# Optimization experiments

Measured on AMD Instinct MI355X. Metric: run time of the kernel, lower is better.

The kernel has to match this reference:

```python
import jax, jax.numpy as jnp
import numpy as np

N_NODES = 50000
N_EDGES = 800000
D = 128
L = 3


def setup_inputs() -> dict:
    key = jax.random.key(0)
    ks = jax.random.split(key, 16)
    x = jax.random.normal(ks[0], (N_NODES, D), dtype=jnp.float32)
    edge_index = jax.random.randint(ks[1], (2, N_EDGES), 0, N_NODES, dtype=jnp.int32)
    # ensure every node has at least one incoming edge (degree > 0)
    edge_index = edge_index.at[1, :N_NODES].set(jnp.arange(N_NODES, dtype=jnp.int32))
    edge_attr = jax.random.normal(ks[2], (N_EDGES, 1), dtype=jnp.float32)
    s = 1.0 / np.sqrt(D)
    lin_w = jax.random.normal(ks[3], (L, 1, D), dtype=jnp.float32)          # edge_dim=1 -> D
    lin_b = jax.random.normal(ks[4], (L, D), dtype=jnp.float32) * s
    eps = jnp.zeros((L,), dtype=jnp.float32)                                 # initial_eps = 0, trainable
    w1 = jax.random.normal(ks[5], (L, D, D), dtype=jnp.float32) * s
    b1 = jax.random.normal(ks[6], (L, D), dtype=jnp.float32) * s
    w2 = jax.random.normal(ks[7], (L, D, D), dtype=jnp.float32) * s
    b2 = jax.random.normal(ks[8], (L, D), dtype=jnp.float32) * s
    d_cat = D + L * D
    final_w = jax.random.normal(ks[9], (d_cat, D), dtype=jnp.float32) / np.sqrt(d_cat)
    final_b = jax.random.normal(ks[10], (D,), dtype=jnp.float32) * s
    return {"x": x, "edge_index": edge_index, "edge_attr": edge_attr,
            "lin_w": lin_w, "lin_b": lin_b, "eps": eps,
            "w1": w1, "b1": b1, "w2": w2, "b2": b2,
            "final_w": final_w, "final_b": final_b}


def reference(x, edge_index, edge_attr, lin_w, lin_b, eps, w1, b1, w2, b2, final_w, final_b):
    src, tgt = edge_index[0], edge_index[1]
    n = x.shape[0]
    # degree of target nodes (float), shape [N, 1]
    deg = jax.ops.segment_sum(jnp.ones(src.shape[0], x.dtype), tgt, num_segments=n)[:, None]
    xs = [x]
    h = x
    for l in range(L):
        e = edge_attr @ lin_w[l] + lin_b[l]                  # [E, D] edge-feature projection
        msg = jax.nn.relu(h[src] + e)                        # gather + fuse + relu
        agg = jax.ops.segment_sum(msg, tgt, num_segments=n)  # scatter-add
        out = agg / deg + (1.0 + eps[l]) * h                 # degree-normalize + eps-residual
        h = jax.nn.relu(out @ w1[l] + b1[l]) @ w2[l] + b2[l] # 2-layer MLP (no BN, no dropout)
        xs.append(h)
    cat = jnp.concatenate(xs, axis=-1)                       # [N, D + L*D]
    return cat @ final_w + final_b
```

## Files before the change

kernel.cpp:

```cpp
#include <hip/hip_runtime.h>

#define NN 50000
#define NE 800000
#define DIM 128
#define NLAYERS 3

typedef __attribute__((ext_vector_type(8))) short bf16x8;
typedef __attribute__((ext_vector_type(4))) float f32x4;

__device__ __forceinline__ unsigned short f2bf_hi(float f) {
    unsigned int u = __float_as_uint(f);
    u += 0x7FFF + ((u >> 16) & 1);
    return (unsigned short)(u >> 16);
}
__device__ __forceinline__ float bf2f(unsigned short u) {
    return __uint_as_float(((unsigned int)u) << 16);
}

__global__ __launch_bounds__(256) void rank_kernel(const int* __restrict__ tgt,
                                                   int* __restrict__ counts,
                                                   int* __restrict__ rank, int E) {
    int base = (blockIdx.x * 256 + threadIdx.x) * 4;
    if (base >= E) return;
    int4 t = *(const int4*)(tgt + base);
    int4 r;
    r.x = atomicAdd(&counts[t.x], 1);
    r.y = atomicAdd(&counts[t.y], 1);
    r.z = atomicAdd(&counts[t.z], 1);
    r.w = atomicAdd(&counts[t.w], 1);
    *(int4*)(rank + base) = r;
}

__global__ __launch_bounds__(256) void scan_partial_kernel(const int* __restrict__ counts,
                                                           int* __restrict__ psum, int n) {
    __shared__ int ws[4];
    int b = blockIdx.x, t = threadIdx.x;
    int idx = b * 1024 + t * 4;
    int v = 0;
    if (idx < n) {
        int4 c = *(const int4*)(counts + idx);
        v = c.x + c.y + c.z + c.w;
    }
#pragma unroll
    for (int o = 32; o > 0; o >>= 1) v += __shfl_xor(v, o);
    int lane = t & 63, wid = t >> 6;
    if (lane == 0) ws[wid] = v;
    __syncthreads();
    if (t == 0) psum[b] = ws[0] + ws[1] + ws[2] + ws[3];
}

__global__ __launch_bounds__(64) void scan_small_kernel(const int* __restrict__ psum,
                                                        int* __restrict__ pbase,
                                                        int* __restrict__ offsets,
                                                        int nb, int n) {
    int lane = threadIdx.x;
    int v = (lane < nb) ? psum[lane] : 0;
    int incl = v;
#pragma unroll
    for (int o = 1; o < 64; o <<= 1) {
        int t = __shfl_up(incl, o);
        if (lane >= o) incl += t;
    }
    if (lane < nb) pbase[lane] = incl - v;
    if (lane == 63) offsets[n] = incl;
}

__global__ __launch_bounds__(256) void scan_apply_kernel(const int* __restrict__ counts,
                                                         const int* __restrict__ pbase,
                                                         int* __restrict__ offsets, int n) {
    __shared__ int ws[4];
    int b = blockIdx.x, t = threadIdx.x;
    int lane = t & 63, wid = t >> 6;
    int idx = b * 1024 + t * 4;
    int4 c = make_int4(0, 0, 0, 0);
    if (idx < n) c = *(const int4*)(counts + idx);
    int tsum = c.x + c.y + c.z + c.w;
    int incl = tsum;
#pragma unroll
    for (int o = 1; o < 64; o <<= 1) {
        int tt = __shfl_up(incl, o);
        if (lane >= o) incl += tt;
    }
    if (lane == 63) ws[wid] = incl;
    __syncthreads();
    int wbase = pbase[b];
    for (int w = 0; w < wid; w++) wbase += ws[w];
    if (idx < n) {
        int e0 = wbase + incl - tsum;
        int4 o;
        o.x = e0;
        o.y = e0 + c.x;
        o.z = o.y + c.y;
        o.w = o.z + c.z;
        *(int4*)(offsets + idx) = o;
    }
}

__global__ __launch_bounds__(256) void scatter2_kernel(
    const int* __restrict__ src, const int* __restrict__ tgt,
    const float* __restrict__ ea, const int* __restrict__ rank,
    const int* __restrict__ offsets, int2* __restrict__ sedge, int E) {
    int base = (blockIdx.x * 256 + threadIdx.x) * 4;
    if (base >= E) return;
    int4 s = *(const int4*)(src + base);
    int4 t = *(const int4*)(tgt + base);
    int4 r = *(const int4*)(rank + base);
    float4 a = *(const float4*)(ea + base);
    sedge[offsets[t.x] + r.x] = make_int2(s.x << 8, __float_as_int(a.x));
    sedge[offsets[t.y] + r.y] = make_int2(s.y << 8, __float_as_int(a.y));
    sedge[offsets[t.z] + r.z] = make_int2(s.z << 8, __float_as_int(a.z));
    sedge[offsets[t.w] + r.w] = make_int2(s.w << 8, __float_as_int(a.w));
}

__global__ __launch_bounds__(256) void xcvt_kernel(const float* __restrict__ x,
                                                   unsigned short* __restrict__ xb, int n) {
    int i = (blockIdx.x * 256 + threadIdx.x) * 4;
    if (i >= n) return;
    float4 v = *(const float4*)(x + i);
    ushort4 o;
    o.x = f2bf_hi(v.x); o.y = f2bf_hi(v.y);
    o.z = f2bf_hi(v.z); o.w = f2bf_hi(v.w);
    *(ushort4*)(xb + i) = o;
}

__global__ __launch_bounds__(256) void agg_kernel(
    const unsigned short* __restrict__ hprev, const int* __restrict__ offs,
    const int2* __restrict__ sedge,
    const float* __restrict__ lw, const float* __restrict__ lb,
    const float* __restrict__ epsp, int layer,
    unsigned short* __restrict__ aggh, unsigned short* __restrict__ aggl, int N) {
    int wv = threadIdx.x >> 6;
    int node = blockIdx.x * 4 + wv;
    if (node >= N) return;
    int lane = threadIdx.x & 63;
    int q = lane >> 4, r = lane & 15;
    int d0 = r * 8;
    float lwv[8], lbv[8];
    *(float4*)&lwv[0] = *(const float4*)(lw + d0);
    *(float4*)&lwv[4] = *(const float4*)(lw + d0 + 4);
    *(float4*)&lbv[0] = *(const float4*)(lb + d0);
    *(float4*)&lbv[4] = *(const float4*)(lb + d0 + 4);
    int s0 = offs[node], s1 = offs[node + 1];
    int cnt = s1 - s0;
    float a[8];
#pragma unroll
    for (int c = 0; c < 8; c++) a[c] = 0.f;

    const char* hbase = (const char*)hprev + r * 16;

    int idx = s0 + q;
    int2 e0 = sedge[min(idx, s1 - 1)];
    int2 e1 = sedge[min(idx + 4, s1 - 1)];
    int2 e2 = sedge[min(idx + 8, s1 - 1)];
    uint4 h0 = *(const uint4*)(hbase + (unsigned)e0.x);
    uint4 h1 = *(const uint4*)(hbase + (unsigned)e1.x);

    for (int it = idx; it < s1; it += 4) {
        uint4 h2 = *(const uint4*)(hbase + (unsigned)e2.x);
        int2 e3 = sedge[min(it + 12, s1 - 1)];
        float wgt = __int_as_float(e0.y);
        unsigned uu[4] = {h0.x, h0.y, h0.z, h0.w};
#pragma unroll
        for (int c = 0; c < 4; c++) {
            float f0 = __uint_as_float(uu[c] << 16);
            float f1 = __uint_as_float(uu[c] & 0xffff0000u);
            a[2 * c]     += fmaxf(f0 + fmaf(wgt, lwv[2 * c], lbv[2 * c]), 0.f);
            a[2 * c + 1] += fmaxf(f1 + fmaf(wgt, lwv[2 * c + 1], lbv[2 * c + 1]), 0.f);
        }
        e0 = e1; e1 = e2; e2 = e3;
        h0 = h1; h1 = h2;
    }

#pragma unroll
    for (int c = 0; c < 8; c++) {
        a[c] += __shfl_xor(a[c], 16);
        a[c] += __shfl_xor(a[c], 32);
    }

    if (q == 0) {
        float inv = 1.f / (float)cnt;
        float ge = 1.f + epsp[layer];
        uint4 hs = *(const uint4*)(hbase + ((unsigned)node << 8));
        unsigned su[4] = {hs.x, hs.y, hs.z, hs.w};
        unsigned short hh[8], hl[8];
#pragma unroll
        for (int c = 0; c < 4; c++) {
            float f0 = __uint_as_float(su[c] << 16);
            float f1 = __uint_as_float(su[c] & 0xffff0000u);
            float v0 = a[2 * c] * inv + ge * f0;
            float v1 = a[2 * c + 1] * inv + ge * f1;
            unsigned short h0v = f2bf_hi(v0), h1v = f2bf_hi(v1);
            hh[2 * c] = h0v; hh[2 * c + 1] = h1v;
            hl[2 * c] = f2bf_hi(v0 - bf2f(h0v));
            hl[2 * c + 1] = f2bf_hi(v1 - bf2f(h1v));
        }
        unsigned short* ph = aggh + (size_t)node * DIM + d0;
        unsigned short* pl = aggl + (size_t)node * DIM + d0;
        *(ushort4*)ph       = *(const ushort4*)&hh[0];
        *(ushort4*)(ph + 4) = *(const ushort4*)&hh[4];
        *(ushort4*)pl       = *(const ushort4*)&hl[0];
        *(ushort4*)(pl + 4) = *(const ushort4*)&hl[4];
    }
}

__device__ __forceinline__ int packidx(int k, int c) {
    return (((k >> 5) << 3) + (c >> 4)) * 512 + (((k >> 3) & 3) << 7) + ((c & 15) << 3) + (k & 7);
}

__global__ __launch_bounds__(256) void wprep_kernel(
    const float* __restrict__ w1, const float* __restrict__ w2, const float* __restrict__ fw,
    unsigned short* __restrict__ w1t_h, unsigned short* __restrict__ w1t_l,
    unsigned short* __restrict__ w2t_h, unsigned short* __restrict__ w2t_l,
    unsigned short* __restrict__ fwt_h, unsigned short* __restrict__ fwt_l) {
    int gid = blockIdx.x * 256 + threadIdx.x;
    float v; int oidx;
    unsigned short *oh, *ol;
    if (gid < 49152) {
        int l = gid >> 14, rem = gid & 16383, k = rem >> 7, c = rem & 127;
        v = w1[gid]; oidx = l * 16384 + packidx(k, c); oh = w1t_h; ol = w1t_l;
    } else if (gid < 98304) {
        int g = gid - 49152;
        int l = g >> 14, rem = g & 16383, k = rem >> 7, c = rem & 127;
        v = w2[g]; oidx = l * 16384 + packidx(k, c); oh = w2t_h; ol = w2t_l;
    } else if (gid < 163840) {
        int g = gid - 98304;
        int k = g >> 7, c = g & 127;
        v = fw[g]; oidx = packidx(k, c); oh = fwt_h; ol = fwt_l;
    } else return;
    unsigned short h = f2bf_hi(v);
    float lo = v - bf2f(h);
    oh[oidx] = h;
    ol[oidx] = f2bf_hi(lo);
}

#define HSTR 136

__global__ __launch_bounds__(256, 4) void mlp_fused(
    const unsigned short* __restrict__ ah_g, const unsigned short* __restrict__ al_g,
    const unsigned short* __restrict__ w1h, const unsigned short* __restrict__ w1l,
    const float* __restrict__ b1,
    const unsigned short* __restrict__ w2h, const unsigned short* __restrict__ w2l,
    const float* __restrict__ b2,
    unsigned short* __restrict__ out, int N) {
    __shared__ unsigned short s_hh[64 * HSTR], s_hl[64 * HSTR];
    int tid = threadIdx.x;
    int lane = tid & 63, w = tid >> 6;
    int q = lane >> 4, lr = lane & 15;
    int wr = w >> 1, wc = w & 1;
    int n0 = blockIdx.x * 64;
    int nb0 = n0 + wc * 32 + lr;

    f32x4 acc[4][2];
#pragma unroll
    for (int i = 0; i < 4; i++)
#pragma unroll
        for (int j = 0; j < 2; j++) acc[i][j] = (f32x4)(0.f);

#pragma unroll
    for (int k0 = 0; k0 < 128; k0 += 32) {
        bf16x8 Bh[2], Bl[2];
#pragma unroll
        for (int j = 0; j < 2; j++) {
            size_t ro = (size_t)min(nb0 + j * 16, N - 1) * DIM + k0 + q * 8;
            Bh[j] = *(const bf16x8*)(ah_g + ro);
            Bl[j] = *(const bf16x8*)(al_g + ro);
        }
#pragma unroll
        for (int i = 0; i < 4; i++) {
            size_t co = ((size_t)((k0 >> 5) * 8 + wr * 4 + i) << 9) + lane * 8;
            bf16x8 Ah = *(const bf16x8*)(w1h + co);
            bf16x8 Al = *(const bf16x8*)(w1l + co);
#pragma unroll
            for (int j = 0; j < 2; j++) {
                acc[i][j] = __builtin_amdgcn_mfma_f32_16x16x32_bf16(Ah, Bh[j], acc[i][j], 0, 0, 0);
                acc[i][j] = __builtin_amdgcn_mfma_f32_16x16x32_bf16(Ah, Bl[j], acc[i][j], 0, 0, 0);
                acc[i][j] = __builtin_amdgcn_mfma_f32_16x16x32_bf16(Al, Bh[j], acc[i][j], 0, 0, 0);
            }
        }
    }

#pragma unroll
    for (int i = 0; i < 4; i++) {
        int hc0 = wr * 64 + i * 16 + q * 4;
        float4 bv = *(const float4*)(b1 + hc0);
        float bvr[4] = {bv.x, bv.y, bv.z, bv.w};
#pragma unroll
        for (int j = 0; j < 2; j++) {
            int nl = wc * 32 + j * 16 + lr;
            unsigned short hh[4], hl[4];
#pragma unroll
            for (int r = 0; r < 4; r++) {
                float v = fmaxf(acc[i][j][r] + bvr[r], 0.f);
                unsigned short h = f2bf_hi(v);
                hh[r] = h;
                hl[r] = f2bf_hi(v - bf2f(h));
            }
            *(ushort4*)&s_hh[nl * HSTR + hc0] = *(const ushort4*)&hh[0];
            *(ushort4*)&s_hl[nl * HSTR + hc0] = *(const ushort4*)&hl[0];
        }
    }
    __syncthreads();

#pragma unroll
    for (int i = 0; i < 4; i++)
#pragma unroll
        for (int j = 0; j < 2; j++) acc[i][j] = (f32x4)(0.f);

#pragma unroll
    for (int k0 = 0; k0 < 128; k0 += 32) {
        bf16x8 Bh[2], Bl[2];
#pragma unroll
        for (int j = 0; j < 2; j++) {
            int so = (wc * 32 + j * 16 + lr) * HSTR + k0 + q * 8;
            Bh[j] = *(const bf16x8*)&s_hh[so];
            Bl[j] = *(const bf16x8*)&s_hl[so];
        }
#pragma unroll
        for (int i = 0; i < 4; i++) {
            size_t co = ((size_t)((k0 >> 5) * 8 + wr * 4 + i) << 9) + lane * 8;
            bf16x8 Ah = *(const bf16x8*)(w2h + co);
            bf16x8 Al = *(const bf16x8*)(w2l + co);
#pragma unroll
            for (int j = 0; j < 2; j++) {
                acc[i][j] = __builtin_amdgcn_mfma_f32_16x16x32_bf16(Ah, Bh[j], acc[i][j], 0, 0, 0);
                acc[i][j] = __builtin_amdgcn_mfma_f32_16x16x32_bf16(Ah, Bl[j], acc[i][j], 0, 0, 0);
                acc[i][j] = __builtin_amdgcn_mfma_f32_16x16x32_bf16(Al, Bh[j], acc[i][j], 0, 0, 0);
            }
        }
    }

#pragma unroll
    for (int i = 0; i < 4; i++) {
        int hc0 = wr * 64 + i * 16 + q * 4;
        float4 bv = *(const float4*)(b2 + hc0);
        float bvr[4] = {bv.x, bv.y, bv.z, bv.w};
#pragma unroll
        for (int j = 0; j < 2; j++) {
            int node = nb0 + j * 16;
            if (node < N) {
                unsigned short o[4];
#pragma unroll
                for (int r = 0; r < 4; r++) o[r] = f2bf_hi(acc[i][j][r] + bvr[r]);
                *(ushort4*)&out[(size_t)node * DIM + hc0] = *(const ushort4*)&o[0];
            }
        }
    }
}

__global__ __launch_bounds__(256, 4) void final_mfma(
    const unsigned short* __restrict__ a0, const unsigned short* __restrict__ a1,
    const unsigned short* __restrict__ a2, const unsigned short* __restrict__ a3,
    const unsigned short* __restrict__ wh, const unsigned short* __restrict__ wl,
    const float* __restrict__ bias, float* __restrict__ out, int N) {
    int tid = threadIdx.x;
    int lane = tid & 63, w = tid >> 6;
    int q = lane >> 4, lr = lane & 15;
    int wr = w >> 1, wc = w & 1;
    int n0 = blockIdx.x * 64;
    int nb0 = n0 + wc * 32 + lr;

    f32x4 acc[4][2];
#pragma unroll
    for (int i = 0; i < 4; i++)
#pragma unroll
        for (int j = 0; j < 2; j++) acc[i][j] = (f32x4)(0.f);

#pragma unroll
    for (int s = 0; s < 4; s++) {
        const unsigned short* asrc = (s == 0) ? a0 : (s == 1) ? a1 : (s == 2) ? a2 : a3;
#pragma unroll
        for (int kk = 0; kk < 128; kk += 32) {
            int k0 = s * 128 + kk;
            bf16x8 B[2];
#pragma unroll
            for (int j = 0; j < 2; j++) {
                size_t ro = (size_t)min(nb0 + j * 16, N - 1) * DIM + kk + q * 8;
                B[j] = *(const bf16x8*)(asrc + ro);
            }
#pragma unroll
            for (int i = 0; i < 4; i++) {
                size_t co = ((size_t)((k0 >> 5) * 8 + wr * 4 + i) << 9) + lane * 8;
                bf16x8 Ah = *(const bf16x8*)(wh + co);
                bf16x8 Al = *(const bf16x8*)(wl + co);
#pragma unroll
                for (int j = 0; j < 2; j++) {
                    acc[i][j] = __builtin_amdgcn_mfma_f32_16x16x32_bf16(Ah, B[j], acc[i][j], 0, 0, 0);
                    acc[i][j] = __builtin_amdgcn_mfma_f32_16x16x32_bf16(Al, B[j], acc[i][j], 0, 0, 0);
                }
            }
        }
    }

#pragma unroll
    for (int i = 0; i < 4; i++) {
        int hc0 = wr * 64 + i * 16 + q * 4;
        float4 bv = *(const float4*)(bias + hc0);
        float bvr[4] = {bv.x, bv.y, bv.z, bv.w};
#pragma unroll
        for (int j = 0; j < 2; j++) {
            int node = nb0 + j * 16;
            if (node < N) {
                float4 o;
                o.x = acc[i][j][0] + bvr[0];
                o.y = acc[i][j][1] + bvr[1];
                o.z = acc[i][j][2] + bvr[2];
                o.w = acc[i][j][3] + bvr[3];
                *(float4*)&out[(size_t)node * DIM + hc0] = o;
            }
        }
    }
}

extern "C" void kernel_launch(void* const* d_in, const int* in_sizes, int n_in,
                              void* d_out, int out_size, void* d_ws, size_t ws_size,
                              hipStream_t stream) {
    const float* x   = (const float*)d_in[0];
    const int* edge_index = (const int*)d_in[1];
    const float* ea  = (const float*)d_in[2];
    const float* lw  = (const float*)d_in[3];
    const float* lb  = (const float*)d_in[4];
    const float* eps = (const float*)d_in[5];
    const float* w1  = (const float*)d_in[6];
    const float* b1  = (const float*)d_in[7];
    const float* w2  = (const float*)d_in[8];
    const float* b2  = (const float*)d_in[9];
    const float* fw  = (const float*)d_in[10];
    const float* fb  = (const float*)d_in[11];
    float* out = (float*)d_out;

    const int N = NN, E = NE;
    const int* src = edge_index;
    const int* tgt = edge_index + E;
    const int NB = (N + 1023) / 1024;

    char* ws = (char*)d_ws;
    size_t off = 0;
    auto alloc = [&](size_t bytes) {
        void* p = ws + off;
        off += (bytes + 255) & ~(size_t)255;
        return p;
    };
    int*   counts  = (int*)alloc((size_t)N * 4);
    int*   offsets = (int*)alloc((size_t)(N + 1) * 4);
    int*   rank    = (int*)alloc((size_t)E * 4);
    int*   psum    = (int*)alloc((size_t)NB * 4);
    int*   pbase   = (int*)alloc((size_t)NB * 4);
    int2*  sedge   = (int2*)alloc((size_t)E * 8);
    unsigned short* w1t_h = (unsigned short*)alloc(49152 * 2);
    unsigned short* w1t_l = (unsigned short*)alloc(49152 * 2);
    unsigned short* w2t_h = (unsigned short*)alloc(49152 * 2);
    unsigned short* w2t_l = (unsigned short*)alloc(49152 * 2);
    unsigned short* fwt_h = (unsigned short*)alloc(65536 * 2);
    unsigned short* fwt_l = (unsigned short*)alloc(65536 * 2);
    unsigned short* xb    = (unsigned short*)alloc((size_t)N * DIM * 2);
    unsigned short* hbuf[3];
    for (int i = 0; i < 3; i++) hbuf[i] = (unsigned short*)alloc((size_t)N * DIM * 2);
    unsigned short* aggh = (unsigned short*)alloc((size_t)N * DIM * 2);
    unsigned short* aggl = (unsigned short*)alloc((size_t)N * DIM * 2);
    (void)ws_size; (void)in_sizes; (void)n_in; (void)out_size;

    hipMemsetAsync(counts, 0, (size_t)N * 4, stream);
    rank_kernel<<<(E / 4 + 255) / 256, 256, 0, stream>>>(tgt, counts, rank, E);
    wprep_kernel<<<640, 256, 0, stream>>>(w1, w2, fw, w1t_h, w1t_l, w2t_h, w2t_l, fwt_h, fwt_l);
    xcvt_kernel<<<(N * DIM / 4 + 255) / 256, 256, 0, stream>>>(x, xb, N * DIM);
    scan_partial_kernel<<<NB, 256, 0, stream>>>(counts, psum, N);
    scan_small_kernel<<<1, 64, 0, stream>>>(psum, pbase, offsets, NB, N);
    scan_apply_kernel<<<NB, 256, 0, stream>>>(counts, pbase, offsets, N);
    scatter2_kernel<<<(E / 4 + 255) / 256, 256, 0, stream>>>(src, tgt, ea, rank, offsets, sedge, E);

    const int GB = (N + 63) / 64;
    for (int l = 0; l < NLAYERS; l++) {
        const unsigned short* hin = (l == 0) ? xb : hbuf[l - 1];
        agg_kernel<<<(N + 3) / 4, 256, 0, stream>>>(hin, offsets, sedge,
            lw + l * DIM, lb + l * DIM, eps, l, aggh, aggl, N);
        mlp_fused<<<GB, 256, 0, stream>>>(
            aggh, aggl,
            w1t_h + l * 16384, w1t_l + l * 16384, b1 + l * DIM,
            w2t_h + l * 16384, w2t_l + l * 16384, b2 + l * DIM,
            hbuf[l], N);
    }
    final_mfma<<<GB, 256, 0, stream>>>(
        xb, hbuf[0], hbuf[1], hbuf[2], fwt_h, fwt_l, fb, out, N);
}
```

Measured before the change: 371.4 us.

## Fuse edge aggregation into MLP kernel via swizzled shared-memory tile

The separate aggregation kernel is merged into the per-layer MLP kernel. Each block now aggregates its 64 nodes straight into shared memory, using 16 threads per node and a 4-deep software pipeline over edges. This removes the global round trip of the hi/lo aggregated buffers and one launch per layer. The padded shared-memory stride is replaced with an XOR swizzle. The cost is that each node's edges are walked serially by one 16-lane group instead of four, so latency hiding and load balance across high-degree nodes may suffer, and occupancy is tied to the MLP's launch bounds.

```diff
diff --git a/kernel.cpp b/kernel.cpp
--- a/kernel.cpp
+++ b/kernel.cpp
@@ -121,86 +121,6 @@
     o.x = f2bf_hi(v.x); o.y = f2bf_hi(v.y);
     o.z = f2bf_hi(v.z); o.w = f2bf_hi(v.w);
     *(ushort4*)(xb + i) = o;
-}
-
-__global__ __launch_bounds__(256) void agg_kernel(
-    const unsigned short* __restrict__ hprev, const int* __restrict__ offs,
-    const int2* __restrict__ sedge,
-    const float* __restrict__ lw, const float* __restrict__ lb,
-    const float* __restrict__ epsp, int layer,
-    unsigned short* __restrict__ aggh, unsigned short* __restrict__ aggl, int N) {
-    int wv = threadIdx.x >> 6;
-    int node = blockIdx.x * 4 + wv;
-    if (node >= N) return;
-    int lane = threadIdx.x & 63;
-    int q = lane >> 4, r = lane & 15;
-    int d0 = r * 8;
-    float lwv[8], lbv[8];
-    *(float4*)&lwv[0] = *(const float4*)(lw + d0);
-    *(float4*)&lwv[4] = *(const float4*)(lw + d0 + 4);
-    *(float4*)&lbv[0] = *(const float4*)(lb + d0);
-    *(float4*)&lbv[4] = *(const float4*)(lb + d0 + 4);
-    int s0 = offs[node], s1 = offs[node + 1];
-    int cnt = s1 - s0;
-    float a[8];
-#pragma unroll
-    for (int c = 0; c < 8; c++) a[c] = 0.f;
-
-    const char* hbase = (const char*)hprev + r * 16;
-
-    int idx = s0 + q;
-    int2 e0 = sedge[min(idx, s1 - 1)];
-    int2 e1 = sedge[min(idx + 4, s1 - 1)];
-    int2 e2 = sedge[min(idx + 8, s1 - 1)];
-    uint4 h0 = *(const uint4*)(hbase + (unsigned)e0.x);
-    uint4 h1 = *(const uint4*)(hbase + (unsigned)e1.x);
-
-    for (int it = idx; it < s1; it += 4) {
-        uint4 h2 = *(const uint4*)(hbase + (unsigned)e2.x);
-        int2 e3 = sedge[min(it + 12, s1 - 1)];
-        float wgt = __int_as_float(e0.y);
-        unsigned uu[4] = {h0.x, h0.y, h0.z, h0.w};
-#pragma unroll
-        for (int c = 0; c < 4; c++) {
-            float f0 = __uint_as_float(uu[c] << 16);
-            float f1 = __uint_as_float(uu[c] & 0xffff0000u);
-            a[2 * c]     += fmaxf(f0 + fmaf(wgt, lwv[2 * c], lbv[2 * c]), 0.f);
-            a[2 * c + 1] += fmaxf(f1 + fmaf(wgt, lwv[2 * c + 1], lbv[2 * c + 1]), 0.f);
-        }
-        e0 = e1; e1 = e2; e2 = e3;
-        h0 = h1; h1 = h2;
-    }
-
-#pragma unroll
-    for (int c = 0; c < 8; c++) {
-        a[c] += __shfl_xor(a[c], 16);
-        a[c] += __shfl_xor(a[c], 32);
-    }
-
-    if (q == 0) {
-        float inv = 1.f / (float)cnt;
-        float ge = 1.f + epsp[layer];
-        uint4 hs = *(const uint4*)(hbase + ((unsigned)node << 8));
-        unsigned su[4] = {hs.x, hs.y, hs.z, hs.w};
-        unsigned short hh[8], hl[8];
-#pragma unroll
-        for (int c = 0; c < 4; c++) {
-            float f0 = __uint_as_float(su[c] << 16);
-            float f1 = __uint_as_float(su[c] & 0xffff0000u);
-            float v0 = a[2 * c] * inv + ge * f0;
-            float v1 = a[2 * c + 1] * inv + ge * f1;
-            unsigned short h0v = f2bf_hi(v0), h1v = f2bf_hi(v1);
-            hh[2 * c] = h0v; hh[2 * c + 1] = h1v;
-            hl[2 * c] = f2bf_hi(v0 - bf2f(h0v));
-            hl[2 * c + 1] = f2bf_hi(v1 - bf2f(h1v));
-        }
-        unsigned short* ph = aggh + (size_t)node * DIM + d0;
-        unsigned short* pl = aggl + (size_t)node * DIM + d0;
-        *(ushort4*)ph       = *(const ushort4*)&hh[0];
-        *(ushort4*)(ph + 4) = *(const ushort4*)&hh[4];
-        *(ushort4*)pl       = *(const ushort4*)&hl[0];
-        *(ushort4*)(pl + 4) = *(const ushort4*)&hl[4];
-    }
 }
 
 __device__ __forceinline__ int packidx(int k, int c) {
@@ -233,21 +153,96 @@
     ol[oidx] = f2bf_hi(lo);
 }
 
-#define HSTR 136
-
-__global__ __launch_bounds__(256, 4) void mlp_fused(
-    const unsigned short* __restrict__ ah_g, const unsigned short* __restrict__ al_g,
+__device__ __forceinline__ int swz(int nl, int h) {
+    return nl * 128 + ((((h >> 3) ^ (nl & 7))) << 3) + (h & 7);
+}
+
+__global__ __launch_bounds__(256, 4) void layer_fused(
+    const unsigned short* __restrict__ hprev, const int* __restrict__ offs,
+    const int2* __restrict__ sedge,
+    const float* __restrict__ lw, const float* __restrict__ lb,
+    const float* __restrict__ epsp, int layer,
     const unsigned short* __restrict__ w1h, const unsigned short* __restrict__ w1l,
     const float* __restrict__ b1,
     const unsigned short* __restrict__ w2h, const unsigned short* __restrict__ w2l,
     const float* __restrict__ b2,
     unsigned short* __restrict__ out, int N) {
-    __shared__ unsigned short s_hh[64 * HSTR], s_hl[64 * HSTR];
+    __shared__ unsigned short s_hh[64 * 128], s_hl[64 * 128];
     int tid = threadIdx.x;
+    int n0 = blockIdx.x * 64;
+
+    {
+        int g = tid >> 4;
+        int r = tid & 15;
+        int d0 = r * 8;
+        float lwv[8], lbv[8];
+        *(float4*)&lwv[0] = *(const float4*)(lw + d0);
+        *(float4*)&lwv[4] = *(const float4*)(lw + d0 + 4);
+        *(float4*)&lbv[0] = *(const float4*)(lb + d0);
+        *(float4*)&lbv[4] = *(const float4*)(lb + d0 + 4);
+        float ge = 1.f + epsp[layer];
+        const char* hb = (const char*)hprev + r * 16;
+
+#pragma unroll
+        for (int t = 0; t < 4; t++) {
+            int nl = t * 16 + g;
+            int node = n0 + nl;
+            if (node < N) {
+                int s0 = offs[node], s1 = offs[node + 1];
+                int cnt = s1 - s0;
+                float a[8];
+#pragma unroll
+                for (int c = 0; c < 8; c++) a[c] = 0.f;
+
+                int2 e0 = sedge[s0];
+                int2 e1 = sedge[min(s0 + 1, s1 - 1)];
+                int2 e2 = sedge[min(s0 + 2, s1 - 1)];
+                uint4 h0 = *(const uint4*)(hb + (unsigned)e0.x);
+                uint4 h1 = *(const uint4*)(hb + (unsigned)e1.x);
+                for (int it = s0; it < s1; ++it) {
+                    uint4 h2 = *(const uint4*)(hb + (unsigned)e2.x);
+                    int2 e3 = sedge[min(it + 3, s1 - 1)];
+                    float wgt = __int_as_float(e0.y);
+                    unsigned uu[4] = {h0.x, h0.y, h0.z, h0.w};
+#pragma unroll
+                    for (int c = 0; c < 4; c++) {
+                        float f0 = __uint_as_float(uu[c] << 16);
+                        float f1 = __uint_as_float(uu[c] & 0xffff0000u);
+                        a[2 * c]     += fmaxf(f0 + fmaf(wgt, lwv[2 * c], lbv[2 * c]), 0.f);
+                        a[2 * c + 1] += fmaxf(f1 + fmaf(wgt, lwv[2 * c + 1], lbv[2 * c + 1]), 0.f);
+                    }
+                    e0 = e1; e1 = e2; e2 = e3;
+                    h0 = h1; h1 = h2;
+                }
+
+                float inv = 1.f / (float)cnt;
+                uint4 hs = *(const uint4*)(hb + ((unsigned)node << 8));
+                unsigned su[4] = {hs.x, hs.y, hs.z, hs.w};
+                unsigned short hh[8], hl[8];
+#pragma unroll
+                for (int c = 0; c < 4; c++) {
+                    float f0 = __uint_as_float(su[c] << 16);
+                    float f1 = __uint_as_float(su[c] & 0xffff0000u);
+                    float v0 = a[2 * c] * inv + ge * f0;
+                    float v1 = a[2 * c + 1] * inv + ge * f1;
+                    unsigned short h0v = f2bf_hi(v0), h1v = f2bf_hi(v1);
+                    hh[2 * c] = h0v; hh[2 * c + 1] = h1v;
+                    hl[2 * c] = f2bf_hi(v0 - bf2f(h0v));
+                    hl[2 * c + 1] = f2bf_hi(v1 - bf2f(h1v));
+                }
+                int idx = swz(nl, d0);
+                *(ushort4*)&s_hh[idx]     = *(const ushort4*)&hh[0];
+                *(ushort4*)&s_hh[idx + 4] = *(const ushort4*)&hh[4];
+                *(ushort4*)&s_hl[idx]     = *(const ushort4*)&hl[0];
+                *(ushort4*)&s_hl[idx + 4] = *(const ushort4*)&hl[4];
+            }
+        }
+    }
+    __syncthreads();
+
     int lane = tid & 63, w = tid >> 6;
     int q = lane >> 4, lr = lane & 15;
     int wr = w >> 1, wc = w & 1;
-    int n0 = blockIdx.x * 64;
     int nb0 = n0 + wc * 32 + lr;
 
     f32x4 acc[4][2];
@@ -261,9 +256,9 @@
         bf16x8 Bh[2], Bl[2];
 #pragma unroll
         for (int j = 0; j < 2; j++) {
-            size_t ro = (size_t)min(nb0 + j * 16, N - 1) * DIM + k0 + q * 8;
-            Bh[j] = *(const bf16x8*)(ah_g + ro);
-            Bl[j] = *(const bf16x8*)(al_g + ro);
+            int idx = swz(wc * 32 + j * 16 + lr, k0 + q * 8);
+            Bh[j] = *(const bf16x8*)&s_hh[idx];
+            Bl[j] = *(const bf16x8*)&s_hl[idx];
         }
 #pragma unroll
         for (int i = 0; i < 4; i++) {
@@ -278,6 +273,7 @@
             }
         }
     }
+    __syncthreads();
 
 #pragma unroll
     for (int i = 0; i < 4; i++) {
@@ -295,8 +291,9 @@
                 hh[r] = h;
                 hl[r] = f2bf_hi(v - bf2f(h));
             }
-            *(ushort4*)&s_hh[nl * HSTR + hc0] = *(const ushort4*)&hh[0];
-            *(ushort4*)&s_hl[nl * HSTR + hc0] = *(const ushort4*)&hl[0];
+            int idx = swz(nl, hc0);
+            *(ushort4*)&s_hh[idx] = *(const ushort4*)&hh[0];
+            *(ushort4*)&s_hl[idx] = *(const ushort4*)&hl[0];
         }
     }
     __syncthreads();
@@ -311,9 +308,9 @@
         bf16x8 Bh[2], Bl[2];
 #pragma unroll
         for (int j = 0; j < 2; j++) {
-            int so = (wc * 32 + j * 16 + lr) * HSTR + k0 + q * 8;
-            Bh[j] = *(const bf16x8*)&s_hh[so];
-            Bl[j] = *(const bf16x8*)&s_hl[so];
+            int idx = swz(wc * 32 + j * 16 + lr, k0 + q * 8);
+            Bh[j] = *(const bf16x8*)&s_hh[idx];
+            Bl[j] = *(const bf16x8*)&s_hl[idx];
         }
 #pragma unroll
         for (int i = 0; i < 4; i++) {
@@ -455,8 +452,6 @@
     unsigned short* xb    = (unsigned short*)alloc((size_t)N * DIM * 2);
     unsigned short* hbuf[3];
     for (int i = 0; i < 3; i++) hbuf[i] = (unsigned short*)alloc((size_t)N * DIM * 2);
-    unsigned short* aggh = (unsigned short*)alloc((size_t)N * DIM * 2);
-    unsigned short* aggl = (unsigned short*)alloc((size_t)N * DIM * 2);
     (void)ws_size; (void)in_sizes; (void)n_in; (void)out_size;
 
     hipMemsetAsync(counts, 0, (size_t)N * 4, stream);
@@ -471,10 +466,8 @@
     const int GB = (N + 63) / 64;
     for (int l = 0; l < NLAYERS; l++) {
         const unsigned short* hin = (l == 0) ? xb : hbuf[l - 1];
-        agg_kernel<<<(N + 3) / 4, 256, 0, stream>>>(hin, offsets, sedge,
-            lw + l * DIM, lb + l * DIM, eps, l, aggh, aggl, N);
-        mlp_fused<<<GB, 256, 0, stream>>>(
-            aggh, aggl,
+        layer_fused<<<GB, 256, 0, stream>>>(hin, offsets, sedge,
+            lw + l * DIM, lb + l * DIM, eps, l,
             w1t_h + l * 16384, w1t_l + l * 16384, b1 + l * DIM,
             w2t_h + l * 16384, w2t_l + l * 16384, b2 + l * DIM,
             hbuf[l], N);
```

New measurement: 367.9 us. About the same (-0.9%).

## Assign one node per 16-lane group in aggregation, drop cross-lane reduction

Applied to the files above, without the earlier changes.

The aggregation kernel now maps each node to a 16-thread group, so each wavefront handles four nodes instead of one node split across four edge-strided quarters. Each group walks its node's edge list sequentially with a deeper 3-ahead gather prefetch, and the shuffle reduction plus the single-quarter epilogue are removed. Launch bounds now request higher occupancy. The trade-off is divergence and load imbalance within a wavefront when the four nodes have different degrees, and a longer serial dependency per node.

```diff
diff --git a/kernel.cpp b/kernel.cpp
--- a/kernel.cpp
+++ b/kernel.cpp
@@ -123,41 +123,42 @@
     *(ushort4*)(xb + i) = o;
 }
 
-__global__ __launch_bounds__(256) void agg_kernel(
+__global__ __launch_bounds__(256, 8) void agg_kernel(
     const unsigned short* __restrict__ hprev, const int* __restrict__ offs,
     const int2* __restrict__ sedge,
     const float* __restrict__ lw, const float* __restrict__ lb,
     const float* __restrict__ epsp, int layer,
     unsigned short* __restrict__ aggh, unsigned short* __restrict__ aggl, int N) {
-    int wv = threadIdx.x >> 6;
-    int node = blockIdx.x * 4 + wv;
+    int g = threadIdx.x >> 4;
+    int r = threadIdx.x & 15;
+    int node = blockIdx.x * 16 + g;
     if (node >= N) return;
-    int lane = threadIdx.x & 63;
-    int q = lane >> 4, r = lane & 15;
     int d0 = r * 8;
     float lwv[8], lbv[8];
     *(float4*)&lwv[0] = *(const float4*)(lw + d0);
     *(float4*)&lwv[4] = *(const float4*)(lw + d0 + 4);
     *(float4*)&lbv[0] = *(const float4*)(lb + d0);
     *(float4*)&lbv[4] = *(const float4*)(lb + d0 + 4);
+    const char* hb = (const char*)hprev + r * 16;
+
     int s0 = offs[node], s1 = offs[node + 1];
+    int sm = s1 - 1;
     int cnt = s1 - s0;
     float a[8];
 #pragma unroll
     for (int c = 0; c < 8; c++) a[c] = 0.f;
 
-    const char* hbase = (const char*)hprev + r * 16;
-
-    int idx = s0 + q;
-    int2 e0 = sedge[min(idx, s1 - 1)];
-    int2 e1 = sedge[min(idx + 4, s1 - 1)];
-    int2 e2 = sedge[min(idx + 8, s1 - 1)];
-    uint4 h0 = *(const uint4*)(hbase + (unsigned)e0.x);
-    uint4 h1 = *(const uint4*)(hbase + (unsigned)e1.x);
-
-    for (int it = idx; it < s1; it += 4) {
-        uint4 h2 = *(const uint4*)(hbase + (unsigned)e2.x);
-        int2 e3 = sedge[min(it + 12, s1 - 1)];
+    int2 e0 = sedge[s0];
+    int2 e1 = sedge[min(s0 + 1, sm)];
+    int2 e2 = sedge[min(s0 + 2, sm)];
+    int2 e3 = sedge[min(s0 + 3, sm)];
+    uint4 h0 = *(const uint4*)(hb + (unsigned)e0.x);
+    uint4 h1 = *(const uint4*)(hb + (unsigned)e1.x);
+    uint4 h2 = *(const uint4*)(hb + (unsigned)e2.x);
+
+    for (int it = s0; it < s1; ++it) {
+        uint4 h3 = *(const uint4*)(hb + (unsigned)e3.x);
+        int2 e4 = sedge[min(it + 4, sm)];
         float wgt = __int_as_float(e0.y);
         unsigned uu[4] = {h0.x, h0.y, h0.z, h0.w};
 #pragma unroll
@@ -167,40 +168,32 @@
             a[2 * c]     += fmaxf(f0 + fmaf(wgt, lwv[2 * c], lbv[2 * c]), 0.f);
             a[2 * c + 1] += fmaxf(f1 + fmaf(wgt, lwv[2 * c + 1], lbv[2 * c + 1]), 0.f);
         }
-        e0 = e1; e1 = e2; e2 = e3;
-        h0 = h1; h1 = h2;
-    }
-
-#pragma unroll
-    for (int c = 0; c < 8; c++) {
-        a[c] += __shfl_xor(a[c], 16);
-        a[c] += __shfl_xor(a[c], 32);
-    }
-
-    if (q == 0) {
-        float inv = 1.f / (float)cnt;
-        float ge = 1.f + epsp[layer];
-        uint4 hs = *(const uint4*)(hbase + ((unsigned)node << 8));
-        unsigned su[4] = {hs.x, hs.y, hs.z, hs.w};
-        unsigned short hh[8], hl[8];
-#pragma unroll
-        for (int c = 0; c < 4; c++) {
-            float f0 = __uint_as_float(su[c] << 16);
-            float f1 = __uint_as_float(su[c] & 0xffff0000u);
-            float v0 = a[2 * c] * inv + ge * f0;
-            float v1 = a[2 * c + 1] * inv + ge * f1;
-            unsigned short h0v = f2bf_hi(v0), h1v = f2bf_hi(v1);
-            hh[2 * c] = h0v; hh[2 * c + 1] = h1v;
-            hl[2 * c] = f2bf_hi(v0 - bf2f(h0v));
-            hl[2 * c + 1] = f2bf_hi(v1 - bf2f(h1v));
-        }
-        unsigned short* ph = aggh + (size_t)node * DIM + d0;
-        unsigned short* pl = aggl + (size_t)node * DIM + d0;
-        *(ushort4*)ph       = *(const ushort4*)&hh[0];
-        *(ushort4*)(ph + 4) = *(const ushort4*)&hh[4];
-        *(ushort4*)pl       = *(const ushort4*)&hl[0];
-        *(ushort4*)(pl + 4) = *(const ushort4*)&hl[4];
-    }
+        e0 = e1; e1 = e2; e2 = e3; e3 = e4;
+        h0 = h1; h1 = h2; h2 = h3;
+    }
+
+    float inv = 1.f / (float)cnt;
+    float ge = 1.f + epsp[layer];
+    uint4 hs = *(const uint4*)(hb + ((unsigned)node << 8));
+    unsigned su[4] = {hs.x, hs.y, hs.z, hs.w};
+    unsigned short hh[8], hl[8];
+#pragma unroll
+    for (int c = 0; c < 4; c++) {
+        float f0 = __uint_as_float(su[c] << 16);
+        float f1 = __uint_as_float(su[c] & 0xffff0000u);
+        float v0 = a[2 * c] * inv + ge * f0;
+        float v1 = a[2 * c + 1] * inv + ge * f1;
+        unsigned short h0v = f2bf_hi(v0), h1v = f2bf_hi(v1);
+        hh[2 * c] = h0v; hh[2 * c + 1] = h1v;
+        hl[2 * c] = f2bf_hi(v0 - bf2f(h0v));
+        hl[2 * c + 1] = f2bf_hi(v1 - bf2f(h1v));
+    }
+    unsigned short* ph = aggh + (size_t)node * DIM + d0;
+    unsigned short* pl = aggl + (size_t)node * DIM + d0;
+    *(ushort4*)ph       = *(const ushort4*)&hh[0];
+    *(ushort4*)(ph + 4) = *(const ushort4*)&hh[4];
+    *(ushort4*)pl       = *(const ushort4*)&hl[0];
+    *(ushort4*)(pl + 4) = *(const ushort4*)&hl[4];
 }
 
 __device__ __forceinline__ int packidx(int k, int c) {
@@ -469,9 +462,10 @@
     scatter2_kernel<<<(E / 4 + 255) / 256, 256, 0, stream>>>(src, tgt, ea, rank, offsets, sedge, E);
 
     const int GB = (N + 63) / 64;
+    const int AB = (N + 15) / 16;
     for (int l = 0; l < NLAYERS; l++) {
         const unsigned short* hin = (l == 0) ? xb : hbuf[l - 1];
-        agg_kernel<<<(N + 3) / 4, 256, 0, stream>>>(hin, offsets, sedge,
+        agg_kernel<<<AB, 256, 0, stream>>>(hin, offsets, sedge,
             lw + l * DIM, lb + l * DIM, eps, l, aggh, aggl, N);
         mlp_fused<<<GB, 256, 0, stream>>>(
             aggh, aggl,
```

New measurement: 366.8 us. No clear change (-1.2%).
